# Optimization experiments

Measured on AMD Instinct MI355X. Metric: run time of the kernel, lower is better.

## Reference

```python
import jax, jax.numpy as jnp
import numpy as np

N_NODES = 10000
N_EDGES = 640000
N_GRAPHS = 100
D_FEAT = 128
D_HID = 512


def setup_inputs() -> dict:
    key = jax.random.key(0)
    ks = jax.random.split(key, 6)
    nodes = jax.random.normal(ks[0], (N_NODES, D_FEAT), jnp.float32)
    edges = jax.random.uniform(ks[1], (N_EDGES, 1), jnp.float32)  # per-edge regularization weight
    senders = jax.random.randint(ks[2], (N_EDGES,), 0, N_NODES, jnp.int32)
    receivers = jax.random.randint(ks[3], (N_EDGES,), 0, N_NODES, jnp.int32)
    n_node = jnp.full((N_GRAPHS,), N_NODES // N_GRAPHS, jnp.int32)
    n_edge = jnp.full((N_GRAPHS,), N_EDGES // N_GRAPHS, jnp.int32)
    W1 = jax.random.normal(ks[4], (D_FEAT, D_HID), jnp.float32) / np.float32(np.sqrt(D_FEAT))
    b1 = jnp.zeros((D_HID,), jnp.float32)
    W2 = jax.random.normal(ks[5], (D_HID, D_FEAT), jnp.float32) / np.float32(np.sqrt(D_HID))
    b2 = jnp.zeros((D_FEAT,), jnp.float32)
    return dict(nodes=nodes, edges=edges, senders=senders, receivers=receivers,
                n_node=n_node, n_edge=n_edge, W1=W1, b1=b1, W2=W2, b2=b2)


def reference(nodes, edges, senders, receivers, n_node, n_edge, W1, b1, W2, b2):
    G = n_node.shape[0]
    E = edges.shape[0]
    # graph id for each edge (EdgesToGlobalsAggregator segment ids)
    edge_gid = jnp.repeat(jnp.arange(G, dtype=jnp.int32), n_edge, total_repeat_length=E)
    w = edges[:, 0]  # [E] edge weights
    # example_weights = unsorted_segment_sum of edge features per graph
    example_weights = jax.ops.segment_sum(w, edge_gid, num_segments=G)  # [G]
    # GraphIndependent node model: MLP applied per node
    h = jax.nn.relu(nodes @ W1 + b1) @ W2 + b2  # [N, D]
    # EdgeRelationNetwork edge block: gather sender/receiver features, weighted L2 distance
    src = jnp.take(h, senders, axis=0)     # [E, D]
    dst = jnp.take(h, receivers, axis=0)   # [E, D]
    edge_out = w * jnp.sum(jnp.square(src - dst), axis=-1)  # [E]
    # aggregate edges -> globals (unsorted_segment_sum)
    globals_agg = jax.ops.segment_sum(edge_out, edge_gid, num_segments=G)  # [G]
    # graph loss: mean(divide_no_nan(globals, example_weights))
    graph_loss = jnp.mean(jnp.where(example_weights != 0.0,
                                    globals_agg / jnp.where(example_weights != 0.0, example_weights, 1.0),
                                    0.0))
    # NodeGraphModel output: node features at last node of each graph
    node_ids = jnp.cumsum(n_node) - 1  # [G]
    node_out = jnp.take(h, node_ids, axis=0)  # [G, D]
    return node_out, graph_loss
```

## Files before the change

kernel.cpp:

```cpp
#include <hip/hip_runtime.h>

#define D_F 128
#define D_H 512
#define SHS 520

typedef short v8s __attribute__((ext_vector_type(8)));
typedef float v4f __attribute__((ext_vector_type(4)));

__device__ inline unsigned short f2bf(float f) {
    unsigned u = __float_as_uint(f);
    unsigned r = (u + 0x7fffu + ((u >> 16) & 1u)) >> 16;
    return (unsigned short)r;
}
__device__ inline float bf2f(unsigned short s) {
    return __uint_as_float(((unsigned)s) << 16);
}

__global__ __launch_bounds__(256) void prep_kernel(
    const float* __restrict__ W1, const float* __restrict__ W2,
    const int* __restrict__ n_node, const int* __restrict__ n_edge,
    unsigned short* __restrict__ W1T, unsigned short* __restrict__ W2T,
    int* __restrict__ ec, int* __restrict__ nid,
    float* __restrict__ ew, float* __restrict__ ga, int G, int E)
{
    if (blockIdx.x == 0) {
        __shared__ int sne[512];
        __shared__ int snn[512];
        const int t = threadIdx.x;
        for (int g = t; g < G; g += 256) { sne[g] = n_edge[g]; snn[g] = n_node[g]; }
        __syncthreads();
        for (int g = t; g < G; g += 256) {
            int se = 0, sn = 0;
            for (int k = 0; k < g; ++k)  se += sne[k];
            for (int k = 0; k <= g; ++k) sn += snn[k];
            ec[g]  = se;
            nid[g] = sn - 1;
            ew[g] = 0.f;
            ga[g] = 0.f;
            if (g == G - 1) {
                int tot = se + sne[g];
                ec[G] = tot > E ? tot : E;
            }
        }
    }
    int i = blockIdx.x * 256 + threadIdx.x;
    if (i < D_F * D_H) {
        int n = i >> 7, k = i & (D_F - 1);
        W1T[i] = f2bf(W1[k * D_H + n]);
        int n2 = i >> 9, k2 = i & (D_H - 1);
        W2T[i] = f2bf(W2[k2 * D_F + n2]);
    }
}

__global__ __launch_bounds__(256) void mlp_mfma_kernel(
    const float* __restrict__ nodes,
    const unsigned short* __restrict__ W1T, const float* __restrict__ b1,
    const unsigned short* __restrict__ W2T, const float* __restrict__ b2,
    unsigned short* __restrict__ hbf, int N)
{
    __shared__ unsigned short sH[16 * SHS];

    const int t    = threadIdx.x;
    const int wave = t >> 6;
    const int lane = t & 63;
    const int li   = lane & 15;
    const int quad = lane >> 4;
    const int row0 = blockIdx.x * 16;

    v8s a1[4];
    {
        int r = min(row0 + li, N - 1);
        const float* xp = nodes + (size_t)r * D_F + quad * 8;
        #pragma unroll
        for (int ks = 0; ks < 4; ++ks) {
            float4 f0 = *(const float4*)(xp + ks * 32);
            float4 f1 = *(const float4*)(xp + ks * 32 + 4);
            v8s v;
            v[0] = (short)f2bf(f0.x); v[1] = (short)f2bf(f0.y);
            v[2] = (short)f2bf(f0.z); v[3] = (short)f2bf(f0.w);
            v[4] = (short)f2bf(f1.x); v[5] = (short)f2bf(f1.y);
            v[6] = (short)f2bf(f1.z); v[7] = (short)f2bf(f1.w);
            a1[ks] = v;
        }
    }

    #pragma unroll 2
    for (int jj = 0; jj < 8; ++jj) {
        const int n0 = (wave * 8 + jj) * 16;
        const unsigned short* wp = W1T + (size_t)(n0 + li) * D_F + quad * 8;
        v4f acc = {0.f, 0.f, 0.f, 0.f};
        #pragma unroll
        for (int ks = 0; ks < 4; ++ks) {
            v8s b = *(const v8s*)(wp + ks * 32);
            acc = __builtin_amdgcn_mfma_f32_16x16x32_bf16(a1[ks], b, acc, 0, 0, 0);
        }
        float bias = b1[n0 + li];
        #pragma unroll
        for (int r = 0; r < 4; ++r) {
            float hv = fmaxf(acc[r] + bias, 0.f);
            int m = quad * 4 + r;
            sH[m * SHS + n0 + li] = f2bf(hv);
        }
    }
    __syncthreads();

    v8s aH[16];
    #pragma unroll
    for (int ks = 0; ks < 16; ++ks)
        aH[ks] = *(const v8s*)(sH + li * SHS + ks * 32 + quad * 8);

    #pragma unroll 1
    for (int j2 = 0; j2 < 2; ++j2) {
        const int n0 = (wave * 2 + j2) * 16;
        const unsigned short* wp = W2T + (size_t)(n0 + li) * D_H + quad * 8;
        v4f acc = {0.f, 0.f, 0.f, 0.f};
        #pragma unroll
        for (int kc = 0; kc < 4; ++kc) {
            v8s b0 = *(const v8s*)(wp + (kc * 4 + 0) * 32);
            v8s b1v = *(const v8s*)(wp + (kc * 4 + 1) * 32);
            v8s b2v = *(const v8s*)(wp + (kc * 4 + 2) * 32);
            v8s b3v = *(const v8s*)(wp + (kc * 4 + 3) * 32);
            acc = __builtin_amdgcn_mfma_f32_16x16x32_bf16(aH[kc * 4 + 0], b0,  acc, 0, 0, 0);
            acc = __builtin_amdgcn_mfma_f32_16x16x32_bf16(aH[kc * 4 + 1], b1v, acc, 0, 0, 0);
            acc = __builtin_amdgcn_mfma_f32_16x16x32_bf16(aH[kc * 4 + 2], b2v, acc, 0, 0, 0);
            acc = __builtin_amdgcn_mfma_f32_16x16x32_bf16(aH[kc * 4 + 3], b3v, acc, 0, 0, 0);
        }
        float bias = b2[n0 + li];
        #pragma unroll
        for (int r = 0; r < 4; ++r) {
            int grow = row0 + quad * 4 + r;
            if (grow < N)
                hbf[(size_t)grow * D_F + n0 + li] = f2bf(acc[r] + bias);
        }
    }
}

__global__ __launch_bounds__(256) void edge_kernel(
    const unsigned short* __restrict__ hbf, const float* __restrict__ wedge,
    const int* __restrict__ senders, const int* __restrict__ receivers,
    const int* __restrict__ ec,
    float* __restrict__ ew, float* __restrict__ ga,
    int E, int G)
{
    __shared__ int   sec[513];
    __shared__ float sga[512];
    __shared__ float sew[512];
    const int t = threadIdx.x;
    for (int i = t; i <= G; i += 256) sec[i] = ec[i];
    for (int i = t; i < G;  i += 256) { sga[i] = 0.f; sew[i] = 0.f; }
    __syncthreads();

    const unsigned* __restrict__ h32 = (const unsigned*)hbf;
    const int lane   = t & 63;
    const int wid    = blockIdx.x * 4 + (t >> 6);
    const int nwaves = gridDim.x * 4;
    const int chunk  = (E + nwaves - 1) / nwaves;
    const int e0 = wid * chunk;
    const int e1 = min(E, e0 + chunk);

    if (e0 < e1) {
        int gid;
        { int lo = 0, hi = G - 1;
          while (lo < hi) { int m = (lo + hi + 1) >> 1; if (sec[m] <= e0) lo = m; else hi = m - 1; }
          gid = lo; }

        float accE = 0.f, accW = 0.f;

        for (int tb = e0; tb < e1; tb += 64) {
            const int nt  = min(64, e1 - tb);
            const int ecl = min(tb + lane, e1 - 1);
            const bool vld = (tb + lane) < e1;
            int   sv = __builtin_nontemporal_load(senders + ecl);
            int   rv = __builtin_nontemporal_load(receivers + ecl);
            float wv = vld ? __builtin_nontemporal_load(wedge + ecl) : 0.f;

            if (tb + nt <= sec[gid + 1]) {
                #pragma unroll 1
                for (int i = 0; i < 64; i += 8) {
                    unsigned av[8], bv[8];
                    int su[8], ru[8];
                    #pragma unroll
                    for (int u = 0; u < 8; ++u) {
                        su[u] = __shfl(sv, i + u);
                        ru[u] = __shfl(rv, i + u);
                    }
                    #pragma unroll
                    for (int u = 0; u < 8; ++u) {
                        av[u] = h32[(size_t)su[u] * 64 + lane];
                        bv[u] = h32[(size_t)ru[u] * 64 + lane];
                    }
                    #pragma unroll
                    for (int u = 0; u < 8; ++u) {
                        float w = __shfl(wv, i + u);
                        float alo = __uint_as_float(av[u] << 16);
                        float ahi = __uint_as_float(av[u] & 0xffff0000u);
                        float blo = __uint_as_float(bv[u] << 16);
                        float bhi = __uint_as_float(bv[u] & 0xffff0000u);
                        float dlo = alo - blo, dhi = ahi - bhi;
                        float sq  = fmaf(dlo, dlo, dhi * dhi);
                        accE = fmaf(w, sq, accE);
                        accW += w;
                    }
                }
            } else {
                for (int i = 0; i < nt; ++i) {
                    int e = tb + i;
                    while (e >= sec[gid + 1]) {
                        float rE = accE;
                        #pragma unroll
                        for (int m = 32; m > 0; m >>= 1) rE += __shfl_xor(rE, m);
                        if (lane == 0 && (rE != 0.f || accW != 0.f)) {
                            atomicAdd(&sga[gid], rE);
                            atomicAdd(&sew[gid], accW);
                        }
                        accE = 0.f; accW = 0.f;
                        ++gid;
                    }
                    int   s = __shfl(sv, i);
                    int   r = __shfl(rv, i);
                    float w = __shfl(wv, i);
                    unsigned a = h32[(size_t)s * 64 + lane];
                    unsigned b = h32[(size_t)r * 64 + lane];
                    float alo = __uint_as_float(a << 16);
                    float ahi = __uint_as_float(a & 0xffff0000u);
                    float blo = __uint_as_float(b << 16);
                    float bhi = __uint_as_float(b & 0xffff0000u);
                    float dlo = alo - blo, dhi = ahi - bhi;
                    float sq  = fmaf(dlo, dlo, dhi * dhi);
                    accE = fmaf(w, sq, accE);
                    accW += w;
                }
            }
        }
        float rE = accE;
        #pragma unroll
        for (int m = 32; m > 0; m >>= 1) rE += __shfl_xor(rE, m);
        if (lane == 0 && (rE != 0.f || accW != 0.f)) {
            atomicAdd(&sga[gid], rE);
            atomicAdd(&sew[gid], accW);
        }
    }

    __syncthreads();
    for (int g = t; g < G; g += 256) {
        float vg = sga[g], vw = sew[g];
        if (vg != 0.f || vw != 0.f) {
            atomicAdd(&ga[g], vg);
            atomicAdd(&ew[g], vw);
        }
    }
}

__global__ __launch_bounds__(128) void finalize_kernel(
    const unsigned short* __restrict__ hbf, const int* __restrict__ nid,
    const float* __restrict__ ew, const float* __restrict__ ga,
    float* __restrict__ out, int G)
{
    const int g = blockIdx.x;
    const int t = threadIdx.x;
    if (g < G) {
        int src = nid[g];
        out[(size_t)g * D_F + t] = bf2f(hbf[(size_t)src * D_F + t]);
    } else {
        float p = 0.f;
        for (int i = t; i < G; i += 128) {
            float w = ew[i];
            p += (w != 0.f) ? ga[i] / w : 0.f;
        }
        #pragma unroll
        for (int m = 32; m > 0; m >>= 1) p += __shfl_xor(p, m);
        __shared__ float sp[2];
        if ((t & 63) == 0) sp[t >> 6] = p;
        __syncthreads();
        if (t == 0) out[(size_t)G * D_F] = (sp[0] + sp[1]) / (float)G;
    }
}

extern "C" void kernel_launch(void* const* d_in, const int* in_sizes, int n_in,
                              void* d_out, int out_size, void* d_ws, size_t ws_size,
                              hipStream_t stream) {
    const float* nodes     = (const float*)d_in[0];
    const float* edges     = (const float*)d_in[1];
    const int*   senders   = (const int*)d_in[2];
    const int*   receivers = (const int*)d_in[3];
    const int*   n_node    = (const int*)d_in[4];
    const int*   n_edge    = (const int*)d_in[5];
    const float* W1        = (const float*)d_in[6];
    const float* b1        = (const float*)d_in[7];
    const float* W2        = (const float*)d_in[8];
    const float* b2        = (const float*)d_in[9];

    const int N = in_sizes[0] / D_F;
    const int E = in_sizes[1];
    const int G = in_sizes[4];

    float* out = (float*)d_out;

    unsigned short* hbf = (unsigned short*)d_ws;
    unsigned short* W1T = hbf + (size_t)N * D_F;
    unsigned short* W2T = W1T + (size_t)D_F * D_H;
    int*            ec  = (int*)(W2T + (size_t)D_F * D_H);
    int*            nid = ec + (G + 1);
    float*          ew  = (float*)(nid + G);
    float*          ga  = ew + G;

    prep_kernel<<<(D_F * D_H + 255) / 256, 256, 0, stream>>>(
        W1, W2, n_node, n_edge, W1T, W2T, ec, nid, ew, ga, G, E);

    const int nblk = (N + 15) / 16;
    mlp_mfma_kernel<<<nblk, 256, 0, stream>>>(nodes, W1T, b1, W2T, b2, hbf, N);

    edge_kernel<<<2048, 256, 0, stream>>>(hbf, edges, senders, receivers, ec, ew, ga, E, G);

    finalize_kernel<<<G + 1, 128, 0, stream>>>(hbf, nid, ew, ga, out, G);
}
```

Before: 160.4 us.

## Fuse finalize into edge kernel, widen MLP blocks, use readlane and packed math

Removes the separate finalize launch. The last edge block, found with an atomic counter and threadfence, now writes the node outputs and the loss. The MLP kernel moves to 512 threads so each wave computes fewer columns, and it batches eight W2 loads ahead of the MFMAs. The edge loop uses readlane instead of shfl to broadcast indices and weights, and uses packed two-wide float math. It also accumulates the weight sum once per tile. Risks include the cost of the last-block serialized tail and the extra scalar readlane work.

```diff
diff --git a/kernel.cpp b/kernel.cpp
--- a/kernel.cpp
+++ b/kernel.cpp
@@ -6,6 +6,7 @@
 
 typedef short v8s __attribute__((ext_vector_type(8)));
 typedef float v4f __attribute__((ext_vector_type(4)));
+typedef float v2f __attribute__((ext_vector_type(2)));
 
 __device__ inline unsigned short f2bf(float f) {
     unsigned u = __float_as_uint(f);
@@ -14,6 +15,12 @@
 }
 __device__ inline float bf2f(unsigned short s) {
     return __uint_as_float(((unsigned)s) << 16);
+}
+__device__ inline v2f upk(unsigned x) {
+    v2f r;
+    r[0] = __uint_as_float(x << 16);
+    r[1] = __uint_as_float(x & 0xffff0000u);
+    return r;
 }
 
 __global__ __launch_bounds__(256) void prep_kernel(
@@ -21,12 +28,14 @@
     const int* __restrict__ n_node, const int* __restrict__ n_edge,
     unsigned short* __restrict__ W1T, unsigned short* __restrict__ W2T,
     int* __restrict__ ec, int* __restrict__ nid,
-    float* __restrict__ ew, float* __restrict__ ga, int G, int E)
+    float* __restrict__ ew, float* __restrict__ ga, int* __restrict__ dctr,
+    int G, int E)
 {
     if (blockIdx.x == 0) {
         __shared__ int sne[512];
         __shared__ int snn[512];
         const int t = threadIdx.x;
+        if (t == 0) *dctr = 0;
         for (int g = t; g < G; g += 256) { sne[g] = n_edge[g]; snn[g] = n_node[g]; }
         __syncthreads();
         for (int g = t; g < G; g += 256) {
@@ -52,7 +61,7 @@
     }
 }
 
-__global__ __launch_bounds__(256) void mlp_mfma_kernel(
+__global__ __launch_bounds__(512) void mlp_mfma_kernel(
     const float* __restrict__ nodes,
     const unsigned short* __restrict__ W1T, const float* __restrict__ b1,
     const unsigned short* __restrict__ W2T, const float* __restrict__ b2,
@@ -85,8 +94,8 @@
     }
 
     #pragma unroll 2
-    for (int jj = 0; jj < 8; ++jj) {
-        const int n0 = (wave * 8 + jj) * 16;
+    for (int jj = 0; jj < 4; ++jj) {
+        const int n0 = (wave * 4 + jj) * 16;
         const unsigned short* wp = W1T + (size_t)(n0 + li) * D_F + quad * 8;
         v4f acc = {0.f, 0.f, 0.f, 0.f};
         #pragma unroll
@@ -109,21 +118,19 @@
     for (int ks = 0; ks < 16; ++ks)
         aH[ks] = *(const v8s*)(sH + li * SHS + ks * 32 + quad * 8);
 
-    #pragma unroll 1
-    for (int j2 = 0; j2 < 2; ++j2) {
-        const int n0 = (wave * 2 + j2) * 16;
+    {
+        const int n0 = wave * 16;
         const unsigned short* wp = W2T + (size_t)(n0 + li) * D_H + quad * 8;
         v4f acc = {0.f, 0.f, 0.f, 0.f};
         #pragma unroll
-        for (int kc = 0; kc < 4; ++kc) {
-            v8s b0 = *(const v8s*)(wp + (kc * 4 + 0) * 32);
-            v8s b1v = *(const v8s*)(wp + (kc * 4 + 1) * 32);
-            v8s b2v = *(const v8s*)(wp + (kc * 4 + 2) * 32);
-            v8s b3v = *(const v8s*)(wp + (kc * 4 + 3) * 32);
-            acc = __builtin_amdgcn_mfma_f32_16x16x32_bf16(aH[kc * 4 + 0], b0,  acc, 0, 0, 0);
-            acc = __builtin_amdgcn_mfma_f32_16x16x32_bf16(aH[kc * 4 + 1], b1v, acc, 0, 0, 0);
-            acc = __builtin_amdgcn_mfma_f32_16x16x32_bf16(aH[kc * 4 + 2], b2v, acc, 0, 0, 0);
-            acc = __builtin_amdgcn_mfma_f32_16x16x32_bf16(aH[kc * 4 + 3], b3v, acc, 0, 0, 0);
+        for (int kc = 0; kc < 2; ++kc) {
+            v8s bb[8];
+            #pragma unroll
+            for (int u = 0; u < 8; ++u)
+                bb[u] = *(const v8s*)(wp + (kc * 8 + u) * 32);
+            #pragma unroll
+            for (int u = 0; u < 8; ++u)
+                acc = __builtin_amdgcn_mfma_f32_16x16x32_bf16(aH[kc * 8 + u], bb[u], acc, 0, 0, 0);
         }
         float bias = b2[n0 + li];
         #pragma unroll
@@ -138,13 +145,15 @@
 __global__ __launch_bounds__(256) void edge_kernel(
     const unsigned short* __restrict__ hbf, const float* __restrict__ wedge,
     const int* __restrict__ senders, const int* __restrict__ receivers,
-    const int* __restrict__ ec,
-    float* __restrict__ ew, float* __restrict__ ga,
-    int E, int G)
+    const int* __restrict__ ec, const int* __restrict__ nid,
+    float* __restrict__ ew, float* __restrict__ ga, int* __restrict__ dctr,
+    float* __restrict__ out, int E, int G)
 {
     __shared__ int   sec[513];
     __shared__ float sga[512];
     __shared__ float sew[512];
+    __shared__ int   sLast;
+    __shared__ float sred[4];
     const int t = threadIdx.x;
     for (int i = t; i <= G; i += 256) sec[i] = ec[i];
     for (int i = t; i < G;  i += 256) { sga[i] = 0.f; sew[i] = 0.f; }
@@ -164,80 +173,83 @@
           while (lo < hi) { int m = (lo + hi + 1) >> 1; if (sec[m] <= e0) lo = m; else hi = m - 1; }
           gid = lo; }
 
-        float accE = 0.f, accW = 0.f;
+        v2f  acc2 = {0.f, 0.f};
+        float accW = 0.f;
 
         for (int tb = e0; tb < e1; tb += 64) {
             const int nt  = min(64, e1 - tb);
             const int ecl = min(tb + lane, e1 - 1);
             const bool vld = (tb + lane) < e1;
-            int   sv = __builtin_nontemporal_load(senders + ecl);
-            int   rv = __builtin_nontemporal_load(receivers + ecl);
-            float wv = vld ? __builtin_nontemporal_load(wedge + ecl) : 0.f;
+            int      sv  = __builtin_nontemporal_load(senders + ecl);
+            int      rv  = __builtin_nontemporal_load(receivers + ecl);
+            float    wv  = vld ? __builtin_nontemporal_load(wedge + ecl) : 0.f;
+            unsigned wvi = __float_as_uint(wv);
 
             if (tb + nt <= sec[gid + 1]) {
                 #pragma unroll 1
                 for (int i = 0; i < 64; i += 8) {
-                    unsigned av[8], bv[8];
-                    int su[8], ru[8];
+                    unsigned a[8], b[8];
+                    float    wu[8];
                     #pragma unroll
                     for (int u = 0; u < 8; ++u) {
-                        su[u] = __shfl(sv, i + u);
-                        ru[u] = __shfl(rv, i + u);
+                        int su = __builtin_amdgcn_readlane(sv, i + u);
+                        int ru = __builtin_amdgcn_readlane(rv, i + u);
+                        wu[u]  = __uint_as_float((unsigned)__builtin_amdgcn_readlane((int)wvi, i + u));
+                        const unsigned* pa = h32 + ((size_t)su << 6);
+                        const unsigned* pb = h32 + ((size_t)ru << 6);
+                        a[u] = pa[lane];
+                        b[u] = pb[lane];
                     }
                     #pragma unroll
                     for (int u = 0; u < 8; ++u) {
-                        av[u] = h32[(size_t)su[u] * 64 + lane];
-                        bv[u] = h32[(size_t)ru[u] * 64 + lane];
-                    }
-                    #pragma unroll
-                    for (int u = 0; u < 8; ++u) {
-                        float w = __shfl(wv, i + u);
-                        float alo = __uint_as_float(av[u] << 16);
-                        float ahi = __uint_as_float(av[u] & 0xffff0000u);
-                        float blo = __uint_as_float(bv[u] << 16);
-                        float bhi = __uint_as_float(bv[u] & 0xffff0000u);
-                        float dlo = alo - blo, dhi = ahi - bhi;
-                        float sq  = fmaf(dlo, dlo, dhi * dhi);
-                        accE = fmaf(w, sq, accE);
-                        accW += w;
+                        v2f d  = upk(a[u]) - upk(b[u]);
+                        v2f dd = d * d;
+                        acc2[0] = fmaf(dd[0], wu[u], acc2[0]);
+                        acc2[1] = fmaf(dd[1], wu[u], acc2[1]);
                     }
                 }
+                accW += wv;
             } else {
                 for (int i = 0; i < nt; ++i) {
                     int e = tb + i;
                     while (e >= sec[gid + 1]) {
-                        float rE = accE;
+                        float rE = acc2[0] + acc2[1];
+                        float rW = accW;
                         #pragma unroll
-                        for (int m = 32; m > 0; m >>= 1) rE += __shfl_xor(rE, m);
-                        if (lane == 0 && (rE != 0.f || accW != 0.f)) {
+                        for (int m = 32; m > 0; m >>= 1) {
+                            rE += __shfl_xor(rE, m);
+                            rW += __shfl_xor(rW, m);
+                        }
+                        if (lane == 0 && (rE != 0.f || rW != 0.f)) {
                             atomicAdd(&sga[gid], rE);
-                            atomicAdd(&sew[gid], accW);
+                            atomicAdd(&sew[gid], rW);
                         }
-                        accE = 0.f; accW = 0.f;
+                        acc2[0] = 0.f; acc2[1] = 0.f; accW = 0.f;
                         ++gid;
                     }
-                    int   s = __shfl(sv, i);
-                    int   r = __shfl(rv, i);
-                    float w = __shfl(wv, i);
-                    unsigned a = h32[(size_t)s * 64 + lane];
-                    unsigned b = h32[(size_t)r * 64 + lane];
-                    float alo = __uint_as_float(a << 16);
-                    float ahi = __uint_as_float(a & 0xffff0000u);
-                    float blo = __uint_as_float(b << 16);
-                    float bhi = __uint_as_float(b & 0xffff0000u);
-                    float dlo = alo - blo, dhi = ahi - bhi;
-                    float sq  = fmaf(dlo, dlo, dhi * dhi);
-                    accE = fmaf(w, sq, accE);
-                    accW += w;
+                    int   s = __builtin_amdgcn_readlane(sv, i);
+                    int   r = __builtin_amdgcn_readlane(rv, i);
+                    float w = __uint_as_float((unsigned)__builtin_amdgcn_readlane((int)wvi, i));
+                    const unsigned* pa = h32 + ((size_t)s << 6);
+                    const unsigned* pb = h32 + ((size_t)r << 6);
+                    v2f d  = upk(pa[lane]) - upk(pb[lane]);
+                    v2f dd = d * d;
+                    acc2[0] = fmaf(dd[0], w, acc2[0]);
+                    acc2[1] = fmaf(dd[1], w, acc2[1]);
+                    if (lane == 0) accW += w;
                 }
             }
         }
-        float rE = accE;
-        #pragma unroll
-        for (int m = 32; m > 0; m >>= 1) rE += __shfl_xor(rE, m);
-        if (lane == 0 && (rE != 0.f || accW != 0.f)) {
+        float rE = acc2[0] + acc2[1];
+        float rW = accW;
+        #pragma unroll
+        for (int m = 32; m > 0; m >>= 1) {
+            rE += __shfl_xor(rE, m);
+            rW += __shfl_xor(rW, m);
+        }
+        if (lane == 0 && (rE != 0.f || rW != 0.f)) {
             atomicAdd(&sga[gid], rE);
-            atomicAdd(&sew[gid], accW);
+            atomicAdd(&sew[gid], rW);
         }
     }
 
@@ -249,30 +261,30 @@
             atomicAdd(&ew[g], vw);
         }
     }
-}
-
-__global__ __launch_bounds__(128) void finalize_kernel(
-    const unsigned short* __restrict__ hbf, const int* __restrict__ nid,
-    const float* __restrict__ ew, const float* __restrict__ ga,
-    float* __restrict__ out, int G)
-{
-    const int g = blockIdx.x;
-    const int t = threadIdx.x;
-    if (g < G) {
-        int src = nid[g];
-        out[(size_t)g * D_F + t] = bf2f(hbf[(size_t)src * D_F + t]);
-    } else {
+
+    __threadfence();
+    if (t == 0) sLast = (atomicAdd(dctr, 1) == gridDim.x - 1) ? 1 : 0;
+    __syncthreads();
+    if (sLast) {
+        __threadfence();
+        const int total = G * D_F;
+        for (int i = t; i < total; i += 256) {
+            int g = i >> 7;
+            int c = i & (D_F - 1);
+            out[i] = bf2f(hbf[(size_t)nid[g] * D_F + c]);
+        }
         float p = 0.f;
-        for (int i = t; i < G; i += 128) {
-            float w = ew[i];
-            p += (w != 0.f) ? ga[i] / w : 0.f;
+        for (int g = t; g < G; g += 256) {
+            float w = atomicAdd(&ew[g], 0.f);
+            float v = atomicAdd(&ga[g], 0.f);
+            p += (w != 0.f) ? v / w : 0.f;
         }
         #pragma unroll
         for (int m = 32; m > 0; m >>= 1) p += __shfl_xor(p, m);
-        __shared__ float sp[2];
-        if ((t & 63) == 0) sp[t >> 6] = p;
+        if ((t & 63) == 0) sred[t >> 6] = p;
         __syncthreads();
-        if (t == 0) out[(size_t)G * D_F] = (sp[0] + sp[1]) / (float)G;
+        if (t == 0)
+            out[total] = (sred[0] + sred[1] + sred[2] + sred[3]) / (float)G;
     }
 }
 
@@ -303,14 +315,14 @@
     int*            nid = ec + (G + 1);
     float*          ew  = (float*)(nid + G);
     float*          ga  = ew + G;
+    int*            dctr = (int*)(ga + G);
 
     prep_kernel<<<(D_F * D_H + 255) / 256, 256, 0, stream>>>(
-        W1, W2, n_node, n_edge, W1T, W2T, ec, nid, ew, ga, G, E);
+        W1, W2, n_node, n_edge, W1T, W2T, ec, nid, ew, ga, dctr, G, E);
 
     const int nblk = (N + 15) / 16;
-    mlp_mfma_kernel<<<nblk, 256, 0, stream>>>(nodes, W1T, b1, W2T, b2, hbf, N);
-
-    edge_kernel<<<2048, 256, 0, stream>>>(hbf, edges, senders, receivers, ec, ew, ga, E, G);
-
-    finalize_kernel<<<G + 1, 128, 0, stream>>>(hbf, nid, ew, ga, out, G);
-}
+    mlp_mfma_kernel<<<nblk, 512, 0, stream>>>(nodes, W1T, b1, W2T, b2, hbf, N);
+
+    edge_kernel<<<2048, 256, 0, stream>>>(hbf, edges, senders, receivers, ec, nid,
+                                          ew, ga, dctr, out, E, G);
+}
```

Result: slower. 294.7 us (+83.8%).
